# Performance work log

Hardware: AMD Instinct MI355X
Metric: run time of the kernel (lower is better)

Reference implementation:

```python
import jax, jax.numpy as jnp
from jax import lax
import numpy as np

B, C, H, W = 16, 1, 1024, 1024


def _erode(x, ksize=3):
    # torch: zero-pad then min over ksize x ksize window
    pad = (ksize - 1) // 2
    xp = jnp.pad(x, ((0, 0), (0, 0), (pad, pad), (pad, pad)))  # constant 0, matches F.pad
    return lax.reduce_window(xp, jnp.array(jnp.inf, x.dtype), lax.min,
                             (1, 1, ksize, ksize), (1, 1, 1, 1), 'VALID')


def _circle_weights(y_true):
    e1 = _erode(y_true)
    e2 = _erode(e1)
    e3 = _erode(e2)
    e4 = _erode(e3)
    circle_all = (0.4 * (y_true - e1) + 0.5 * (e1 - e2)
                  + 0.6 * (e2 - e3) + 0.7 * (e3 - e4))
    circle_all = jnp.where(circle_all == 0, jnp.asarray(0.8, circle_all.dtype), circle_all)
    return lax.stop_gradient(circle_all)  # computed under torch.no_grad()


def setup_inputs() -> dict:
    key = jax.random.key(0)
    k1, k2 = jax.random.split(key)
    y_pred = jax.random.uniform(k1, (B, C, H, W), dtype=jnp.float32)
    # binary-ish segmentation mask so erosion rings are non-trivial
    y_true = (jax.random.uniform(k2, (B, C, H, W)) > 0.7).astype(jnp.float32)
    return {"y_pred": y_pred, "y_true": y_true}


def reference(y_pred, y_true):
    w = _circle_weights(y_true)
    loss = (y_pred - y_true) ** 2 * w  # MSELoss(reduction='none') * weights
    return (loss.mean(axis=(1, 2, 3)), loss.mean())
```

## Files before the change

kernel.cpp:

```cpp
#include <hip/hip_runtime.h>
#include <stdint.h>

#define BATCH 16
#define HH 1024
#define WW 1024
#define TH 8
#define HALO 4
#define ROWS (TH + 2*HALO)
#define WORDS (WW/64)
#define WPAD (WORDS + 1)
#define NTHREADS 256
#define NWAVES (NTHREADS/64)
#define TOTAL_WORDS (BATCH * HH * WORDS)
#define NBLOCKS_MSE (BATCH * (HH / TH))

__global__ __launch_bounds__(NTHREADS) void pack_kernel(
    const float* __restrict__ y_true,
    unsigned long long* __restrict__ packed)
{
    const int lane = threadIdx.x & 63;
    const size_t base = ((size_t)((blockIdx.x * NTHREADS + threadIdx.x) >> 6)) * 32;
    unsigned long long mine = 0ull;
    #pragma unroll
    for (int i = 0; i < 32; ++i) {
        float v = y_true[(base + (size_t)i) * 64 + lane];
        unsigned long long m = __ballot(v != 0.0f);
        mine = (lane == i) ? m : mine;
    }
    if (lane < 32) packed[base + lane] = mine;
}

__global__ __launch_bounds__(NTHREADS) void erode_mse_kernel(
    const float* __restrict__ y_pred,
    const unsigned long long* __restrict__ packed,
    float* __restrict__ ws_partial)
{
    __shared__ unsigned long long bits0[ROWS][WPAD];
    __shared__ unsigned long long bufA[ROWS][WPAD];
    __shared__ unsigned long long bufB[ROWS][WPAD];
    __shared__ unsigned long long E[4][TH][WPAD];
    __shared__ float wavesum[NWAVES];

    const int tid  = threadIdx.x;
    const int lane = tid & 63;
    const int wave = tid >> 6;

    const int im = blockIdx.x / (HH / TH);
    const int rb = blockIdx.x % (HH / TH);
    const int r0 = rb * TH - HALO;

    const float* yp = y_pred + (size_t)im * HH * WW;

    float4 pv[TH];
    #pragma unroll
    for (int row = 0; row < TH; ++row) {
        int gr = r0 + HALO + row;
        pv[row] = *reinterpret_cast<const float4*>(&yp[(size_t)gr * WW + tid * 4]);
    }

    {
        int row  = tid >> 4;
        int word = tid & (WORDS - 1);
        int gr   = r0 + row;
        unsigned long long m = 0ull;
        if (gr >= 0 && gr < HH)
            m = packed[((size_t)im * HH + gr) * WORDS + word];
        bits0[row][word] = m;
        bufA[row][word]  = m;
    }
    __syncthreads();

    #pragma unroll
    for (int k = 1; k <= 4; ++k) {
        unsigned long long (*src)[WPAD] = (k & 1) ? bufA : bufB;
        unsigned long long (*dst)[WPAD] = (k & 1) ? bufB : bufA;
        int lo = k, hi = ROWS - k;
        int n  = (hi - lo) * WORDS;
        if (tid < n) {
            int row  = lo + (tid >> 4);
            int word = tid & (WORDS - 1);
            unsigned long long h0, h1, h2;
            {
                unsigned long long m = src[row - 1][word];
                unsigned long long l = (word > 0)         ? src[row - 1][word - 1] : 0ull;
                unsigned long long r = (word < WORDS - 1) ? src[row - 1][word + 1] : 0ull;
                h0 = m & ((m << 1) | (l >> 63)) & ((m >> 1) | (r << 63));
            }
            {
                unsigned long long m = src[row][word];
                unsigned long long l = (word > 0)         ? src[row][word - 1] : 0ull;
                unsigned long long r = (word < WORDS - 1) ? src[row][word + 1] : 0ull;
                h1 = m & ((m << 1) | (l >> 63)) & ((m >> 1) | (r << 63));
            }
            {
                unsigned long long m = src[row + 1][word];
                unsigned long long l = (word > 0)         ? src[row + 1][word - 1] : 0ull;
                unsigned long long r = (word < WORDS - 1) ? src[row + 1][word + 1] : 0ull;
                h2 = m & ((m << 1) | (l >> 63)) & ((m >> 1) | (r << 63));
            }
            unsigned long long res = h0 & h1 & h2;
            dst[row][word] = res;
            if (row >= HALO && row < HALO + TH) E[k - 1][row - HALO][word] = res;
        }
        __syncthreads();
    }

    const int word = tid >> 4;
    const int bsh  = (tid & 15) * 4;
    float lsum = 0.0f;
    #pragma unroll
    for (int row = 0; row < TH; ++row) {
        unsigned int y4 = (unsigned int)((bits0[row + HALO][word] >> bsh) & 0xFull);
        unsigned int n1 = (unsigned int)((E[0][row][word] >> bsh) & 0xFull);
        unsigned int n2 = (unsigned int)((E[1][row][word] >> bsh) & 0xFull);
        unsigned int n3 = (unsigned int)((E[2][row][word] >> bsh) & 0xFull);
        unsigned int n4 = (unsigned int)((E[3][row][word] >> bsh) & 0xFull);
        float pvals[4] = {pv[row].x, pv[row].y, pv[row].z, pv[row].w};
        #pragma unroll
        for (int j = 0; j < 4; ++j) {
            unsigned int y = (y4 >> j) & 1u;
            unsigned int c = y + ((n1 >> j) & 1u) + ((n2 >> j) & 1u)
                               + ((n3 >> j) & 1u) + ((n4 >> j) & 1u);
            float w = (c == 0u || c == 5u) ? 0.8f : (0.3f + 0.1f * (float)c);
            float d = pvals[j] - (float)y;
            lsum += d * d * w;
        }
    }

    for (int off = 32; off > 0; off >>= 1)
        lsum += __shfl_down(lsum, off, 64);
    if (lane == 0) wavesum[wave] = lsum;
    __syncthreads();
    if (tid == 0) {
        float s = 0.0f;
        for (int wv = 0; wv < NWAVES; ++wv) s += wavesum[wv];
        ws_partial[blockIdx.x] = s;
    }
}

__global__ __launch_bounds__(NTHREADS) void reduce_kernel(
    const float* __restrict__ partial,
    float* __restrict__ out)
{
    __shared__ float ssum[NTHREADS];
    __shared__ float imsum[BATCH];
    const int tid = threadIdx.x;
    float s = 0.0f;
    #pragma unroll
    for (int j = 0; j < NBLOCKS_MSE / NTHREADS; ++j)
        s += partial[tid * (NBLOCKS_MSE / NTHREADS) + j];
    ssum[tid] = s;
    __syncthreads();
    if (tid < BATCH) {
        float a = 0.0f;
        #pragma unroll
        for (int t = 0; t < NTHREADS / BATCH; ++t)
            a += ssum[tid * (NTHREADS / BATCH) + t];
        imsum[tid] = a;
        out[tid] = a * (1.0f / (float)(HH * WW));
    }
    __syncthreads();
    if (tid == 0) {
        float tot = 0.0f;
        #pragma unroll
        for (int i = 0; i < BATCH; ++i) tot += imsum[i];
        out[BATCH] = tot * (1.0f / ((float)BATCH * (float)(HH * WW)));
    }
}

__global__ __launch_bounds__(NTHREADS) void circle_mse_kernel(
    const float* __restrict__ y_pred,
    const float* __restrict__ y_true,
    float* __restrict__ out)
{
    __shared__ unsigned long long bits0[ROWS][WPAD];
    __shared__ unsigned long long cur[ROWS][WPAD];
    __shared__ unsigned long long tmp[ROWS][WPAD];
    __shared__ unsigned long long E[4][TH][WPAD];
    __shared__ float wavesum[NWAVES];

    const int tid  = threadIdx.x;
    const int lane = tid & 63;
    const int wave = tid >> 6;
    const int im = blockIdx.x / (HH / TH);
    const int rb = blockIdx.x % (HH / TH);
    const int r0 = rb * TH - HALO;
    const float* yt = y_true + (size_t)im * HH * WW;
    const float* yp = y_pred + (size_t)im * HH * WW;

    #pragma unroll 8
    for (int p = wave; p < ROWS * WORDS; p += NWAVES) {
        int row  = p >> 4;
        int word = p & (WORDS - 1);
        int gr   = r0 + row;
        unsigned long long m = 0ull;
        if (gr >= 0 && gr < HH) {
            float v = yt[(size_t)gr * WW + word * 64 + lane];
            m = __ballot(v != 0.0f);
        }
        if (lane == 0) { bits0[row][word] = m; cur[row][word] = m; }
    }
    __syncthreads();

    for (int k = 1; k <= 4; ++k) {
        int lo = k - 1, hi = ROWS - (k - 1);
        for (int p = tid; p < (hi - lo) * WORDS; p += NTHREADS) {
            int row  = lo + (p >> 4);
            int word = p & (WORDS - 1);
            unsigned long long m = cur[row][word];
            unsigned long long l = (word > 0)         ? cur[row][word - 1] : 0ull;
            unsigned long long r = (word < WORDS - 1) ? cur[row][word + 1] : 0ull;
            tmp[row][word] = m & ((m << 1) | (l >> 63)) & ((m >> 1) | (r << 63));
        }
        __syncthreads();
        lo = k; hi = ROWS - k;
        for (int p = tid; p < (hi - lo) * WORDS; p += NTHREADS) {
            int row  = lo + (p >> 4);
            int word = p & (WORDS - 1);
            unsigned long long res = tmp[row - 1][word] & tmp[row][word] & tmp[row + 1][word];
            cur[row][word] = res;
            if (row >= HALO && row < HALO + TH) E[k - 1][row - HALO][word] = res;
        }
        __syncthreads();
    }

    const int word = tid >> 4;
    const int bsh  = (tid & 15) * 4;
    float lsum = 0.0f;
    #pragma unroll
    for (int row = 0; row < TH; ++row) {
        int gr = r0 + HALO + row;
        float4 pv = *reinterpret_cast<const float4*>(&yp[(size_t)gr * WW + tid * 4]);
        unsigned int y4 = (unsigned int)((bits0[row + HALO][word] >> bsh) & 0xFull);
        unsigned int n1 = (unsigned int)((E[0][row][word] >> bsh) & 0xFull);
        unsigned int n2 = (unsigned int)((E[1][row][word] >> bsh) & 0xFull);
        unsigned int n3 = (unsigned int)((E[2][row][word] >> bsh) & 0xFull);
        unsigned int n4 = (unsigned int)((E[3][row][word] >> bsh) & 0xFull);
        float pvals[4] = {pv.x, pv.y, pv.z, pv.w};
        #pragma unroll
        for (int j = 0; j < 4; ++j) {
            unsigned int y = (y4 >> j) & 1u;
            unsigned int c = y + ((n1 >> j) & 1u) + ((n2 >> j) & 1u)
                               + ((n3 >> j) & 1u) + ((n4 >> j) & 1u);
            float w = (c == 0u || c == 5u) ? 0.8f : (0.3f + 0.1f * (float)c);
            float d = pvals[j] - (float)y;
            lsum += d * d * w;
        }
    }
    for (int off = 32; off > 0; off >>= 1)
        lsum += __shfl_down(lsum, off, 64);
    if (lane == 0) wavesum[wave] = lsum;
    __syncthreads();
    if (tid == 0) {
        float s = 0.0f;
        for (int wv = 0; wv < NWAVES; ++wv) s += wavesum[wv];
        atomicAdd(&out[im], s * (1.0f / (float)(HH * WW)));
        atomicAdd(&out[BATCH], s * (1.0f / ((float)BATCH * (float)(HH * WW))));
    }
}

extern "C" void kernel_launch(void* const* d_in, const int* in_sizes, int n_in,
                              void* d_out, int out_size, void* d_ws, size_t ws_size,
                              hipStream_t stream) {
    const float* y_pred = (const float*)d_in[0];
    const float* y_true = (const float*)d_in[1];
    float* out = (float*)d_out;

    const size_t need = (size_t)TOTAL_WORDS * sizeof(unsigned long long)
                      + (size_t)NBLOCKS_MSE * sizeof(float);
    if (ws_size >= need && d_ws != nullptr) {
        unsigned long long* packed = (unsigned long long*)d_ws;
        float* ws_partial = (float*)(packed + TOTAL_WORDS);
        pack_kernel<<<dim3(TOTAL_WORDS / 32 / NWAVES), NTHREADS, 0, stream>>>(y_true, packed);
        erode_mse_kernel<<<dim3(NBLOCKS_MSE), NTHREADS, 0, stream>>>(y_pred, packed, ws_partial);
        reduce_kernel<<<dim3(1), NTHREADS, 0, stream>>>(ws_partial, out);
    } else {
        hipMemsetAsync(d_out, 0, (size_t)out_size * sizeof(float), stream);
        circle_mse_kernel<<<dim3(NBLOCKS_MSE), NTHREADS, 0, stream>>>(y_pred, y_true, out);
    }
}
```

Measured before the change: 150.1 us.

## Fuse mask bit-packing into erosion kernel, reading y_true directly

Removes the separate pack kernel and its packed workspace; each block now loads y_true floats for its rows plus halo and builds 64-bit mask words in registers before erosion. This saves a kernel launch and the write/read of the packed bitmap. In exchange, halo rows of y_true are re-read by neighbouring blocks (about twice the y_true traffic), and per-thread 256-byte strided loads are less coalesced than the earlier ballot-based packing.

```diff
diff --git a/kernel.cpp b/kernel.cpp
--- a/kernel.cpp
+++ b/kernel.cpp
@@ -11,28 +11,11 @@
 #define WPAD (WORDS + 1)
 #define NTHREADS 256
 #define NWAVES (NTHREADS/64)
-#define TOTAL_WORDS (BATCH * HH * WORDS)
 #define NBLOCKS_MSE (BATCH * (HH / TH))
 
-__global__ __launch_bounds__(NTHREADS) void pack_kernel(
+__global__ __launch_bounds__(NTHREADS) void fused_mse_kernel(
+    const float* __restrict__ y_pred,
     const float* __restrict__ y_true,
-    unsigned long long* __restrict__ packed)
-{
-    const int lane = threadIdx.x & 63;
-    const size_t base = ((size_t)((blockIdx.x * NTHREADS + threadIdx.x) >> 6)) * 32;
-    unsigned long long mine = 0ull;
-    #pragma unroll
-    for (int i = 0; i < 32; ++i) {
-        float v = y_true[(base + (size_t)i) * 64 + lane];
-        unsigned long long m = __ballot(v != 0.0f);
-        mine = (lane == i) ? m : mine;
-    }
-    if (lane < 32) packed[base + lane] = mine;
-}
-
-__global__ __launch_bounds__(NTHREADS) void erode_mse_kernel(
-    const float* __restrict__ y_pred,
-    const unsigned long long* __restrict__ packed,
     float* __restrict__ ws_partial)
 {
     __shared__ unsigned long long bits0[ROWS][WPAD];
@@ -50,23 +33,32 @@
     const int r0 = rb * TH - HALO;
 
     const float* yp = y_pred + (size_t)im * HH * WW;
-
-    float4 pv[TH];
-    #pragma unroll
-    for (int row = 0; row < TH; ++row) {
-        int gr = r0 + HALO + row;
-        pv[row] = *reinterpret_cast<const float4*>(&yp[(size_t)gr * WW + tid * 4]);
-    }
+    const float* yt = y_true + (size_t)im * HH * WW;
 
     {
         int row  = tid >> 4;
         int word = tid & (WORDS - 1);
         int gr   = r0 + row;
         unsigned long long m = 0ull;
-        if (gr >= 0 && gr < HH)
-            m = packed[((size_t)im * HH + gr) * WORDS + word];
+        if (gr >= 0 && gr < HH) {
+            const uint4* src = reinterpret_cast<const uint4*>(yt + (size_t)gr * WW + word * 64);
+            #pragma unroll
+            for (int i = 0; i < 16; ++i) {
+                uint4 q = src[i];
+                unsigned long long nib = (unsigned long long)(
+                    (q.x ? 1u : 0u) | (q.y ? 2u : 0u) | (q.z ? 4u : 0u) | (q.w ? 8u : 0u));
+                m |= nib << (4 * i);
+            }
+        }
         bits0[row][word] = m;
         bufA[row][word]  = m;
+    }
+
+    float4 pv[TH];
+    #pragma unroll
+    for (int row = 0; row < TH; ++row) {
+        int gr = r0 + HALO + row;
+        pv[row] = *reinterpret_cast<const float4*>(&yp[(size_t)gr * WW + tid * 4]);
     }
     __syncthreads();
 
@@ -266,13 +258,10 @@
     const float* y_true = (const float*)d_in[1];
     float* out = (float*)d_out;
 
-    const size_t need = (size_t)TOTAL_WORDS * sizeof(unsigned long long)
-                      + (size_t)NBLOCKS_MSE * sizeof(float);
+    const size_t need = (size_t)NBLOCKS_MSE * sizeof(float);
     if (ws_size >= need && d_ws != nullptr) {
-        unsigned long long* packed = (unsigned long long*)d_ws;
-        float* ws_partial = (float*)(packed + TOTAL_WORDS);
-        pack_kernel<<<dim3(TOTAL_WORDS / 32 / NWAVES), NTHREADS, 0, stream>>>(y_true, packed);
-        erode_mse_kernel<<<dim3(NBLOCKS_MSE), NTHREADS, 0, stream>>>(y_pred, packed, ws_partial);
+        float* ws_partial = (float*)d_ws;
+        fused_mse_kernel<<<dim3(NBLOCKS_MSE), NTHREADS, 0, stream>>>(y_pred, y_true, ws_partial);
         reduce_kernel<<<dim3(1), NTHREADS, 0, stream>>>(ws_partial, out);
     } else {
         hipMemsetAsync(d_out, 0, (size_t)out_size * sizeof(float), stream);
```

Result: no change. 151.6 us (+1.0%).
